# Kernel optimization log

Hardware: AMD Instinct MI355X
Metric: run time of the kernel (lower is better)

The kernel has to match this reference:

```python
import jax, jax.numpy as jnp
import numpy as np

LOG8 = float(np.log(8.0))


def setup_inputs() -> dict:
    key = jax.random.key(0)
    ks = jax.random.split(key, 5)
    B, T, D = 4, 4096, 1024
    s = 1.0 / float(np.sqrt(D))  # torch default Linear init scale
    return {
        "x": jax.random.normal(ks[0], (B, T, D), dtype=jnp.float32),
        "h": jnp.zeros((B, D), dtype=jnp.float32),
        "W_r": jax.random.uniform(ks[1], (D, D), jnp.float32, -s, s),
        "b_r": jax.random.uniform(ks[2], (D,), jnp.float32, -4.0, -2.0),
        "W_i": jax.random.uniform(ks[3], (D, D), jnp.float32, -s, s),
        "b_i": jnp.zeros((D,), dtype=jnp.float32),
        "W_x": jax.random.uniform(ks[4], (D, D), jnp.float32, -s, s),
    }


def reference(x, h, W_r, b_r, W_i, b_i, W_x):
    # x: (B, T, D); torch Linear is y = x @ W.T + b with W of shape (out, in)
    r = jax.nn.sigmoid(jnp.einsum('btd,ed->bte', x, W_r) + b_r)   # recurrence gate
    i = jax.nn.sigmoid(jnp.einsum('btd,ed->bte', x, W_i) + b_i)   # input gate
    a = jnp.exp(-jax.nn.softplus(LOG8 * r))                        # data-dependent decay in (0,1)
    gate = jnp.sqrt(jnp.clip(1.0 - a * a, 1e-6))
    u = gate * (i * jnp.einsum('btd,ed->bte', x, W_x))             # per-step input term

    # diagonal linear recurrence h_t = a_t * h_{t-1} + u_t, scanned over time
    def step(h_prev, au):
        a_t, u_t = au  # each (B, D)
        h_new = a_t * h_prev + u_t
        return h_new, h_new

    a_t = jnp.swapaxes(a, 0, 1)  # (T, B, D)
    u_t = jnp.swapaxes(u, 0, 1)
    h_last, out = jax.lax.scan(step, h, (a_t, u_t))
    output = jnp.swapaxes(out, 0, 1)  # (B, T, D)
    return output, h_last
```

## Files before the change

### kernel.cpp

```cpp
#include <hip/hip_runtime.h>
#include <stdint.h>

#define D_DIM 1024
#define T_DIM 4096
#define B_DIM 4
#define M_DIM 16384
#define NX 16777216UL
#define NW 1048576UL
#define LOG8F 2.0794415416798357f
#define CHUNK_L 64
#define NCHUNK 64
#define WARM 16
#define NT 32

typedef __attribute__((ext_vector_type(4))) float f32x4;
typedef __attribute__((ext_vector_type(8))) short bf16x8;

__device__ __forceinline__ unsigned short f2bf(float f) {
    unsigned u = __float_as_uint(f);
    u += 0x7fffu + ((u >> 16) & 1u);
    return (unsigned short)(u >> 16);
}
__device__ __forceinline__ float unp_lo(unsigned p) { return __uint_as_float(p << 16); }
__device__ __forceinline__ float unp_hi(unsigned p) { return __uint_as_float(p & 0xffff0000u); }
__device__ __forceinline__ float sigm(float x) { return 1.0f / (1.0f + __expf(-x)); }

__device__ __forceinline__ void gl_lds16(const void* g, void* l) {
    __builtin_amdgcn_global_load_lds(
        (const __attribute__((address_space(1))) void*)g,
        (__attribute__((address_space(3))) void*)l, 16, 0, 0);
}

__global__ __launch_bounds__(256) void cvt_kernel(
    const float* __restrict__ x, const float* __restrict__ Wr,
    const float* __restrict__ Wi, const float* __restrict__ Wx,
    unsigned short* __restrict__ xb, unsigned short* __restrict__ wb)
{
    size_t tid = (size_t)blockIdx.x * 256 + threadIdx.x;
    size_t i = tid * 4;
    const float* src;
    unsigned short* dst;
    size_t off;
    if (i < NX) {
        src = x; dst = xb; off = i;
    } else {
        size_t j = i - NX;
        size_t w = j >> 20;
        off = j & (NW - 1);
        src = (w == 0) ? Wr : (w == 1 ? Wi : Wx);
        dst = wb + w * NW;
    }
    float4 v = *(const float4*)(src + off);
    ushort4 o;
    o.x = f2bf(v.x); o.y = f2bf(v.y); o.z = f2bf(v.z); o.w = f2bf(v.w);
    *(ushort4*)(dst + off) = o;
}

__global__ __launch_bounds__(512, 2) void fused_gemm(
    const unsigned short* __restrict__ xb, const unsigned short* __restrict__ wb,
    const float* __restrict__ b_r, const float* __restrict__ b_i,
    unsigned short* __restrict__ a_out, float* __restrict__ u_out)
{
    __shared__ __align__(16) unsigned short lds[4][16384];

    const int tid  = threadIdx.x;
    const int lane = tid & 63;
    const int wave = tid >> 6;
    const int wm = wave & 1;
    const int wn = wave >> 1;
    const int m0 = ((int)blockIdx.x >> 3) * 128;
    const int d0 = ((int)blockIdx.x & 7) * 128;
    const int frow = lane & 15;
    const int kgrp = lane >> 4;

    const int r0 = tid >> 2;
    const int cgs = (tid & 3) ^ ((r0 >> 1) & 3);
    const unsigned short* srcA  = xb + (size_t)(m0 + r0) * D_DIM + cgs * 8;
    const unsigned short* srcB0 = wb + (size_t)(d0 + r0) * D_DIM + cgs * 8;
    const unsigned short* srcB1 = srcB0 + NW;
    const unsigned short* srcB2 = srcB0 + 2 * NW;

    int offA[4], offB[3][2];
    #pragma unroll
    for (int i = 0; i < 4; i++) {
        const int row = wm * 64 + i * 16 + frow;
        offA[i] = row * 32 + ((kgrp ^ ((row >> 1) & 3)) << 3);
    }
    #pragma unroll
    for (int w = 0; w < 3; w++)
        #pragma unroll
        for (int j = 0; j < 2; j++) {
            const int row = wn * 32 + j * 16 + frow;
            offB[w][j] = (1 + w) * 4096 + row * 32 + ((kgrp ^ ((row >> 1) & 3)) << 3);
        }

    f32x4 acc[3][4][2];
    #pragma unroll
    for (int w = 0; w < 3; w++)
        #pragma unroll
        for (int i = 0; i < 4; i++)
            #pragma unroll
            for (int j = 0; j < 2; j++) acc[w][i][j] = (f32x4){0.f, 0.f, 0.f, 0.f};

    auto stage = [&](int t) {
        const int buf = t & 3;
        const int k0 = t << 5;
        gl_lds16(srcA  + k0, &lds[buf][tid * 8]);
        gl_lds16(srcB0 + k0, &lds[buf][4096 + tid * 8]);
        gl_lds16(srcB1 + k0, &lds[buf][8192 + tid * 8]);
        gl_lds16(srcB2 + k0, &lds[buf][12288 + tid * 8]);
    };

    bf16x8 af_a[4], af_b[4], bf_a[3][2], bf_b[3][2];

    stage(0); stage(1); stage(2);
    asm volatile("s_waitcnt vmcnt(8)" ::: "memory");
    __builtin_amdgcn_s_barrier();
    asm volatile("" ::: "memory");
    #pragma unroll
    for (int i = 0; i < 4; i++) af_a[i] = *(const bf16x8*)&lds[0][offA[i]];
    #pragma unroll
    for (int w = 0; w < 3; w++)
        #pragma unroll
        for (int j = 0; j < 2; j++) bf_a[w][j] = *(const bf16x8*)&lds[0][offB[w][j]];

#define STEP(T, AFC, BFC, AFN, BFN, VM)                                       \
    {                                                                         \
        asm volatile("s_waitcnt vmcnt(" #VM ")" ::: "memory");                \
        __builtin_amdgcn_s_barrier();                                         \
        asm volatile("" ::: "memory");                                        \
        if ((T) + 3 < NT) stage((T) + 3);                                     \
        if ((T) + 1 < NT) {                                                   \
            const unsigned short* nb = lds[((T) + 1) & 3];                    \
            _Pragma("unroll")                                                 \
            for (int i = 0; i < 4; i++)                                       \
                AFN[i] = *(const bf16x8*)&nb[offA[i]];                        \
            _Pragma("unroll")                                                 \
            for (int w = 0; w < 3; w++)                                       \
                _Pragma("unroll")                                             \
                for (int j = 0; j < 2; j++)                                   \
                    BFN[w][j] = *(const bf16x8*)&nb[offB[w][j]];              \
        }                                                                     \
        __builtin_amdgcn_s_setprio(1);                                        \
        _Pragma("unroll")                                                     \
        for (int w = 0; w < 3; w++)                                           \
            _Pragma("unroll")                                                 \
            for (int i = 0; i < 4; i++)                                       \
                _Pragma("unroll")                                             \
                for (int j = 0; j < 2; j++)                                   \
                    acc[w][i][j] = __builtin_amdgcn_mfma_f32_16x16x32_bf16(   \
                        AFC[i], BFC[w][j], acc[w][i][j], 0, 0, 0);            \
        __builtin_amdgcn_s_setprio(0);                                        \
    }

    for (int t = 0; t < 28; t += 2) {
        STEP(t,     af_a, bf_a, af_b, bf_b, 4);
        STEP(t + 1, af_b, bf_b, af_a, bf_a, 4);
    }
    STEP(28, af_a, bf_a, af_b, bf_b, 4);
    STEP(29, af_b, bf_b, af_a, bf_a, 4);
    STEP(30, af_a, bf_a, af_b, bf_b, 0);
    STEP(31, af_b, bf_b, af_a, bf_a, 0);
#undef STEP

    const int mb = m0 + wm * 64 + kgrp * 4;
    const int db = d0 + wn * 32 + frow;
    #pragma unroll
    for (int j = 0; j < 2; j++) {
        const int d = db + j * 16;
        const float br = b_r[d];
        const float bi = b_i[d];
        #pragma unroll
        for (int i = 0; i < 4; i++) {
            const int m = mb + i * 16;
            #pragma unroll
            for (int r = 0; r < 4; r++) {
                const size_t idx = (size_t)(m + r) * D_DIM + d;
                float rg = sigm(acc[0][i][j][r] + br);
                float a = sigm(-LOG8F * rg);
                a_out[idx] = f2bf(a);
                float g = sqrtf(fmaxf(1.0f - a * a, 1e-6f));
                u_out[idx] = g * sigm(acc[1][i][j][r] + bi) * acc[2][i][j][r];
            }
        }
    }
}

__global__ __launch_bounds__(256) void scan_warm(
    const unsigned short* __restrict__ a, const float* __restrict__ u,
    const float* __restrict__ h0, float* __restrict__ hstart)
{
    int tid = blockIdx.x * 256 + threadIdx.x;
    int d = (tid & 511) << 1;
    int bc = tid >> 9;
    int b = bc >> 6;
    int c = bc & (NCHUNK - 1);
    float hx, hy;
    if (c == 0) {
        float2 h = *(const float2*)(h0 + b * D_DIM + d);
        hx = h.x; hy = h.y;
    } else {
        hx = 0.0f; hy = 0.0f;
        size_t base = ((size_t)b * T_DIM + (size_t)c * CHUNK_L - WARM) * D_DIM + d;
        #pragma unroll 4
        for (int t = 0; t < WARM; t++) {
            size_t idx = base + (size_t)t * D_DIM;
            unsigned ap = *(const unsigned*)(a + idx);
            float2 uv = *(const float2*)(u + idx);
            hx = unp_lo(ap) * hx + uv.x;
            hy = unp_hi(ap) * hy + uv.y;
        }
    }
    *(float2*)(hstart + bc * D_DIM + d) = make_float2(hx, hy);
}

__global__ __launch_bounds__(256) void scan_apply(
    const unsigned short* __restrict__ a, const float* __restrict__ hstart,
    float* __restrict__ out)
{
    int tid = blockIdx.x * 256 + threadIdx.x;
    int d = (tid & 511) << 1;
    int bc = tid >> 9;
    int b = bc >> 6;
    int c = bc & (NCHUNK - 1);
    size_t base = ((size_t)b * T_DIM + (size_t)c * CHUNK_L) * D_DIM + d;
    float2 h = *(const float2*)(hstart + bc * D_DIM + d);
    float hx = h.x, hy = h.y;
    #pragma unroll 4
    for (int t = 0; t < CHUNK_L; t++) {
        size_t idx = base + (size_t)t * D_DIM;
        unsigned ap = *(const unsigned*)(a + idx);
        float2 uv = *(const float2*)(out + idx);
        hx = unp_lo(ap) * hx + uv.x;
        hy = unp_hi(ap) * hy + uv.y;
        *(float2*)(out + idx) = make_float2(hx, hy);
    }
    if (c == NCHUNK - 1)
        *(float2*)(out + (size_t)M_DIM * D_DIM + b * D_DIM + d) = make_float2(hx, hy);
}

extern "C" void kernel_launch(void* const* d_in, const int* in_sizes, int n_in,
                              void* d_out, int out_size, void* d_ws, size_t ws_size,
                              hipStream_t stream)
{
    const float* x  = (const float*)d_in[0];
    const float* h0 = (const float*)d_in[1];
    const float* Wr = (const float*)d_in[2];
    const float* br = (const float*)d_in[3];
    const float* Wi = (const float*)d_in[4];
    const float* bi = (const float*)d_in[5];
    const float* Wx = (const float*)d_in[6];
    float* out = (float*)d_out;

    char* ws = (char*)d_ws;
    unsigned short* xb = (unsigned short*)ws;
    unsigned short* wb = (unsigned short*)(ws + 33554432);
    unsigned short* a_buf = (unsigned short*)(ws + 33554432 + 6291456);
    float* hstart = (float*)(ws + 33554432 + 6291456 + 33554432);

    cvt_kernel<<<19456, 256, 0, stream>>>(x, Wr, Wi, Wx, xb, wb);
    fused_gemm<<<1024, 512, 0, stream>>>(xb, wb, br, bi, a_buf, out);
    scan_warm<<<512, 256, 0, stream>>>(a_buf, out, h0, hstart);
    scan_apply<<<512, 256, 0, stream>>>(a_buf, hstart, out);
}
```

Measured before the change: 288.4 us.

## Load weight fragments directly from global into registers, staging only x in LDS

The three weight tiles are no longer staged through shared memory. Each wave now loads its B fragments straight from global memory into registers one k-step ahead, and only the x tile goes through the LDS ring buffer. This cuts LDS capacity and traffic and may raise occupancy. In exchange, each weight element is loaded redundantly by every wave row that uses it, the global loads are less coalesced, and the vmcnt wait counts have to track the mixed load stream.

```diff
diff --git a/kernel.cpp b/kernel.cpp
--- a/kernel.cpp
+++ b/kernel.cpp
@@ -61,7 +61,7 @@
     const float* __restrict__ b_r, const float* __restrict__ b_i,
     unsigned short* __restrict__ a_out, float* __restrict__ u_out)
 {
-    __shared__ __align__(16) unsigned short lds[4][16384];
+    __shared__ __align__(16) unsigned short lds[4][4096];
 
     const int tid  = threadIdx.x;
     const int lane = tid & 63;
@@ -75,24 +75,17 @@
 
     const int r0 = tid >> 2;
     const int cgs = (tid & 3) ^ ((r0 >> 1) & 3);
-    const unsigned short* srcA  = xb + (size_t)(m0 + r0) * D_DIM + cgs * 8;
-    const unsigned short* srcB0 = wb + (size_t)(d0 + r0) * D_DIM + cgs * 8;
-    const unsigned short* srcB1 = srcB0 + NW;
-    const unsigned short* srcB2 = srcB0 + 2 * NW;
-
-    int offA[4], offB[3][2];
+    const unsigned short* srcA = xb + (size_t)(m0 + r0) * D_DIM + cgs * 8;
+
+    const unsigned short* bbase =
+        wb + (size_t)(d0 + wn * 32 + frow) * D_DIM + kgrp * 8;
+
+    int offA[4];
     #pragma unroll
     for (int i = 0; i < 4; i++) {
         const int row = wm * 64 + i * 16 + frow;
         offA[i] = row * 32 + ((kgrp ^ ((row >> 1) & 3)) << 3);
     }
-    #pragma unroll
-    for (int w = 0; w < 3; w++)
-        #pragma unroll
-        for (int j = 0; j < 2; j++) {
-            const int row = wn * 32 + j * 16 + frow;
-            offB[w][j] = (1 + w) * 4096 + row * 32 + ((kgrp ^ ((row >> 1) & 3)) << 3);
-        }
 
     f32x4 acc[3][4][2];
     #pragma unroll
@@ -103,26 +96,26 @@
             for (int j = 0; j < 2; j++) acc[w][i][j] = (f32x4){0.f, 0.f, 0.f, 0.f};
 
     auto stage = [&](int t) {
-        const int buf = t & 3;
-        const int k0 = t << 5;
-        gl_lds16(srcA  + k0, &lds[buf][tid * 8]);
-        gl_lds16(srcB0 + k0, &lds[buf][4096 + tid * 8]);
-        gl_lds16(srcB1 + k0, &lds[buf][8192 + tid * 8]);
-        gl_lds16(srcB2 + k0, &lds[buf][12288 + tid * 8]);
+        gl_lds16(srcA + (t << 5), &lds[t & 3][tid * 8]);
     };
 
+#define LOADB(T, BF)                                                          \
+    _Pragma("unroll")                                                         \
+    for (int w = 0; w < 3; w++)                                               \
+        _Pragma("unroll")                                                     \
+        for (int j = 0; j < 2; j++)                                           \
+            BF[w][j] = *(const bf16x8*)(bbase + (size_t)w * NW +              \
+                                        j * 16 * D_DIM + (T) * 32);
+
     bf16x8 af_a[4], af_b[4], bf_a[3][2], bf_b[3][2];
 
     stage(0); stage(1); stage(2);
-    asm volatile("s_waitcnt vmcnt(8)" ::: "memory");
+    LOADB(0, bf_a);
+    asm volatile("s_waitcnt vmcnt(0)" ::: "memory");
     __builtin_amdgcn_s_barrier();
     asm volatile("" ::: "memory");
     #pragma unroll
     for (int i = 0; i < 4; i++) af_a[i] = *(const bf16x8*)&lds[0][offA[i]];
-    #pragma unroll
-    for (int w = 0; w < 3; w++)
-        #pragma unroll
-        for (int j = 0; j < 2; j++) bf_a[w][j] = *(const bf16x8*)&lds[0][offB[w][j]];
 
 #define STEP(T, AFC, BFC, AFN, BFN, VM)                                       \
     {                                                                         \
@@ -131,15 +124,11 @@
         asm volatile("" ::: "memory");                                        \
         if ((T) + 3 < NT) stage((T) + 3);                                     \
         if ((T) + 1 < NT) {                                                   \
+            LOADB((T) + 1, BFN);                                              \
             const unsigned short* nb = lds[((T) + 1) & 3];                    \
             _Pragma("unroll")                                                 \
             for (int i = 0; i < 4; i++)                                       \
                 AFN[i] = *(const bf16x8*)&nb[offA[i]];                        \
-            _Pragma("unroll")                                                 \
-            for (int w = 0; w < 3; w++)                                       \
-                _Pragma("unroll")                                             \
-                for (int j = 0; j < 2; j++)                                   \
-                    BFN[w][j] = *(const bf16x8*)&nb[offB[w][j]];              \
         }                                                                     \
         __builtin_amdgcn_s_setprio(1);                                        \
         _Pragma("unroll")                                                     \
@@ -153,15 +142,16 @@
         __builtin_amdgcn_s_setprio(0);                                        \
     }
 
-    for (int t = 0; t < 28; t += 2) {
-        STEP(t,     af_a, bf_a, af_b, bf_b, 4);
-        STEP(t + 1, af_b, bf_b, af_a, bf_a, 4);
-    }
-    STEP(28, af_a, bf_a, af_b, bf_b, 4);
-    STEP(29, af_b, bf_b, af_a, bf_a, 4);
-    STEP(30, af_a, bf_a, af_b, bf_b, 0);
+    STEP(0, af_a, bf_a, af_b, bf_b, 1);
+    for (int t = 1; t < 29; t += 2) {
+        STEP(t,     af_b, bf_b, af_a, bf_a, 7);
+        STEP(t + 1, af_a, bf_a, af_b, bf_b, 7);
+    }
+    STEP(29, af_b, bf_b, af_a, bf_a, 7);
+    STEP(30, af_a, bf_a, af_b, bf_b, 6);
     STEP(31, af_b, bf_b, af_a, bf_a, 0);
 #undef STEP
+#undef LOADB
 
     const int mb = m0 + wm * 64 + kgrp * 4;
     const int db = d0 + wn * 32 + frow;
```

Result: slower. 408.0 us (+41.5%).
